# Kernel optimization log

Hardware: AMD Instinct MI355X
Metric: run time of the kernel (lower is better)

The kernel has to match this reference:

```python
import jax, jax.numpy as jnp
import numpy as np

H = W = 14
SENT = H * W  # sentinel label for background (> any real label)
DROP_THR = 0.3
STRIDE = 32


def _min_pool_3x3(labels):
    # labels: [B, H, W] int32; 8-connected neighborhood min (incl. self)
    p = jnp.pad(labels, ((0, 0), (1, 1), (1, 1)), constant_values=SENT)
    shifts = [p[:, i:i + H, j:j + W] for i in range(3) for j in range(3)]
    return jnp.min(jnp.stack(shifts, axis=0), axis=0)


def _label_components(mask):
    # mask: [B, H, W] bool. Iterative min-label propagation (8-connectivity,
    # matching skimage.measure.label default for 2D arrays).
    init = jnp.where(mask, jnp.arange(H * W, dtype=jnp.int32).reshape(1, H, W), SENT)

    def step(_, lab):
        return jnp.where(mask, jnp.minimum(lab, _min_pool_3x3(lab)), SENT)

    # H*W iterations is a safe upper bound on the longest propagation path
    return jax.lax.fori_loop(0, H * W, step, init)


def reference(fms):
    # fms: [B, C, 14, 14]
    attention = jnp.mean(fms, axis=1)                      # [B, H, W] (channel mean)
    max_val = jnp.max(attention.reshape(attention.shape[0], -1), axis=1)  # [B]
    mask = attention > (max_val * DROP_THR)[:, None, None]  # threshold mask

    labels = _label_components(mask)                       # [B, H, W]

    # per-label pixel counts (areas); label ids in [0, H*W)
    lab_flat = labels.reshape(labels.shape[0], -1)          # [B, HW]
    counts = jnp.sum(lab_flat[:, :, None] == jnp.arange(H * W)[None, None, :], axis=1)  # [B, HW]
    # first max -> smallest label id, matching areas.index(max(areas)) in raster order
    best = jnp.argmax(counts, axis=1)                       # [B]
    sel = labels == best[:, None, None]                     # [B, H, W] largest component

    idx = jnp.arange(H)
    row_any = sel.any(axis=2)                               # [B, H]
    col_any = sel.any(axis=1)                               # [B, W]
    min_row = jnp.min(jnp.where(row_any, idx, H), axis=1)
    max_row = jnp.max(jnp.where(row_any, idx, -1), axis=1) + 1  # exclusive, skimage bbox
    min_col = jnp.min(jnp.where(col_any, idx, W), axis=1)
    max_col = jnp.max(jnp.where(col_any, idx, -1), axis=1) + 1

    # empty-mask fallback -> full-image bbox [0, 0, 14, 14]
    empty = jnp.max(counts, axis=1) == 0
    min_row = jnp.where(empty, 0, min_row)
    min_col = jnp.where(empty, 0, min_col)
    max_row = jnp.where(empty, H, max_row)
    max_col = jnp.where(empty, W, max_col)

    x0 = jnp.maximum(min_row * STRIDE - 1, 0)
    y0 = jnp.maximum(min_col * STRIDE - 1, 0)
    x1 = max_row * STRIDE - 1
    y1 = max_col * STRIDE - 1
    return jnp.stack([x0, y0, x1, y1], axis=1).astype(jnp.int32)  # [B, 4]


def setup_inputs() -> dict:
    key = jax.random.key(0)
    fms = jax.random.uniform(key, (64, 2048, 14, 14), dtype=jnp.float32)
    return {"fms": fms}
```

## Files before the change

### kernel.cpp

```cpp
#include <hip/hip_runtime.h>

#define HH 14
#define WW 14
#define P 196
#define CTOT 2048
#define NCHUNK 16
#define CCHUNK 128
#define Q4 49

__global__ __launch_bounds__(256) void chansum_kernel(const float* __restrict__ fms,
                                                      float* __restrict__ partials) {
    const int blk = blockIdx.x;
    const int b = blk >> 4;
    const int k = blk & 15;
    const float4* __restrict__ base =
        (const float4*)(fms + ((size_t)b * CTOT + (size_t)k * CCHUNK) * P);

    __shared__ float lds[5 * P];
    const int t = threadIdx.x;

    if (t < 5 * Q4) {
        const int q = t % Q4;
        const int r = t / Q4;
        float4 acc = {0.f, 0.f, 0.f, 0.f};
        #pragma unroll 4
        for (int c = r; c < CCHUNK; c += 5) {
            float4 v = base[c * Q4 + q];
            acc.x += v.x; acc.y += v.y; acc.z += v.z; acc.w += v.w;
        }
        const int o = r * P + q * 4;
        lds[o + 0] = acc.x; lds[o + 1] = acc.y;
        lds[o + 2] = acc.z; lds[o + 3] = acc.w;
    }
    __syncthreads();
    if (t < P) {
        float s = lds[t] + lds[P + t] + lds[2 * P + t] + lds[3 * P + t] + lds[4 * P + t];
        partials[(size_t)blk * P + t] = s;
    }
}

__global__ __launch_bounds__(256) void bbox_kernel(const float* __restrict__ partials,
                                                   int* __restrict__ out) {
    const int b = blockIdx.x;
    const int t = threadIdx.x;

    __shared__ float redf[4];
    __shared__ unsigned long long ball[4];

    float a = -1e30f;
    if (t < P) {
        const float* pb = partials + (size_t)b * NCHUNK * P + t;
        a = 0.f;
        #pragma unroll
        for (int k = 0; k < NCHUNK; ++k) a += pb[k * P];
    }

    float mx = a;
    #pragma unroll
    for (int off = 32; off >= 1; off >>= 1) mx = fmaxf(mx, __shfl_xor(mx, off));
    if ((t & 63) == 0) redf[t >> 6] = mx;
    __syncthreads();
    const float maxv = fmaxf(fmaxf(redf[0], redf[1]), fmaxf(redf[2], redf[3]));

    const bool maskp = (t < P) && (a > maxv * 0.3f);
    const unsigned long long wb = __ballot(maskp);
    if ((t & 63) == 0) ball[t >> 6] = wb;
    __syncthreads();
    if (t >= 64) return;

    const unsigned long long B0 = ball[0], B1 = ball[1], B2 = ball[2], B3 = ball[3];

    if (B0 == ~0ull && B1 == ~0ull && B2 == ~0ull && (B3 & 0xFull) == 0xFull) {
        if (t == 0) {
            out[b * 4 + 0] = 0;
            out[b * 4 + 1] = 0;
            out[b * 4 + 2] = HH * 32 - 1;
            out[b * 4 + 3] = WW * 32 - 1;
        }
        return;
    }

    const int l = t;
    unsigned rem = 0;
    if (l < HH) {
        const int start = WW * l, w = start >> 6, off = start & 63;
        const unsigned long long Barr[4] = {B0, B1, B2, B3};
        unsigned long long v = Barr[w] >> off;
        if (off + WW > 64) v |= Barr[w + 1] << (64 - off);
        rem = (unsigned)v & 0x3FFFu;
    }

    unsigned bestRow = 0;
    int bestA = 0;

    for (;;) {
        const unsigned long long rb = __ballot(rem != 0);
        if (rb == 0) break;
        const int sr = __ffsll(rb) - 1;
        unsigned reach = (l == sr) ? (rem & (unsigned)(-(int)rem)) : 0u;

        for (;;) {
            const unsigned h = reach | (reach << 1) | (reach >> 1);
            const unsigned up = __shfl_up(h, 1);
            const unsigned dn = __shfl_down(h, 1);
            const unsigned nv = (h | up | dn) & rem;
            const bool chg = (nv != reach);
            reach = nv;
            if (!__any(chg)) break;
        }

        int area = __popc(reach);
        #pragma unroll
        for (int off = 32; off >= 1; off >>= 1) area += __shfl_xor(area, off);
        if (area > bestA) { bestA = area; bestRow = reach; }
        rem &= ~reach;
    }

    int mnr, mxr, mnc, mxc;
    if (bestA == 0) {
        mnr = 0; mxr = HH - 1; mnc = 0; mxc = WW - 1;
    } else {
        const unsigned long long rowb = __ballot(bestRow != 0);
        mnr = __ffsll(rowb) - 1;
        mxr = 63 - __clzll(rowb);
        unsigned cols = bestRow;
        #pragma unroll
        for (int off = 32; off >= 1; off >>= 1) cols |= __shfl_xor(cols, off);
        mnc = __ffs(cols) - 1;
        mxc = 31 - __clz(cols);
    }
    if (l == 0) {
        out[b * 4 + 0] = max(mnr * 32 - 1, 0);
        out[b * 4 + 1] = max(mnc * 32 - 1, 0);
        out[b * 4 + 2] = (mxr + 1) * 32 - 1;
        out[b * 4 + 3] = (mxc + 1) * 32 - 1;
    }
}

extern "C" void kernel_launch(void* const* d_in, const int* in_sizes, int n_in,
                              void* d_out, int out_size, void* d_ws, size_t ws_size,
                              hipStream_t stream) {
    const float* fms = (const float*)d_in[0];
    int* out = (int*)d_out;
    float* partials = (float*)d_ws;

    chansum_kernel<<<dim3(64 * NCHUNK), dim3(256), 0, stream>>>(fms, partials);
    bbox_kernel<<<dim3(64), dim3(256), 0, stream>>>(partials, out);
}
```

Baseline: 22.67 us.

## Fuse channel-sum and bbox kernels via last-block atomic counter

```diff
diff --git a/kernel.cpp b/kernel.cpp
--- a/kernel.cpp
+++ b/kernel.cpp
@@ -8,8 +8,14 @@
 #define CCHUNK 128
 #define Q4 49
 
-__global__ __launch_bounds__(256) void chansum_kernel(const float* __restrict__ fms,
-                                                      float* __restrict__ partials) {
+
+typedef unsigned long long u64;
+union pk2 { float2 f; u64 u; };
+
+__global__ __launch_bounds__(256) void fused_kernel(const float* __restrict__ fms,
+                                                    unsigned* __restrict__ counters,
+                                                    float* __restrict__ partials,
+                                                    int* __restrict__ out) {
     const int blk = blockIdx.x;
     const int b = blk >> 4;
     const int k = blk & 15;
@@ -17,6 +23,11 @@
         (const float4*)(fms + ((size_t)b * CTOT + (size_t)k * CCHUNK) * P);
 
     __shared__ float lds[5 * P];
+    __shared__ float att[P];
+    __shared__ float redf[4];
+    __shared__ unsigned long long ball[4];
+    __shared__ unsigned oldv;
+
     const int t = threadIdx.x;
 
     if (t < 5 * Q4) {
@@ -33,27 +44,36 @@
         lds[o + 2] = acc.z; lds[o + 3] = acc.w;
     }
     __syncthreads();
-    if (t < P) {
-        float s = lds[t] + lds[P + t] + lds[2 * P + t] + lds[3 * P + t] + lds[4 * P + t];
-        partials[(size_t)blk * P + t] = s;
+    if (t < P / 2) {
+        const int p0 = 2 * t;
+        pk2 v;
+        v.f.x = lds[p0]     + lds[P + p0]     + lds[2 * P + p0]     + lds[3 * P + p0]     + lds[4 * P + p0];
+        v.f.y = lds[p0 + 1] + lds[P + p0 + 1] + lds[2 * P + p0 + 1] + lds[3 * P + p0 + 1] + lds[4 * P + p0 + 1];
+        __hip_atomic_store((u64*)(partials + (size_t)blk * P) + t, v.u,
+                           __ATOMIC_RELAXED, __HIP_MEMORY_SCOPE_AGENT);
     }
-}
+    asm volatile("s_waitcnt vmcnt(0)" ::: "memory");
+    __syncthreads();
+    if (t == 0)
+        oldv = __hip_atomic_fetch_add(&counters[b], 1u,
+                                      __ATOMIC_RELAXED, __HIP_MEMORY_SCOPE_AGENT);
+    __syncthreads();
+    if ((oldv & 15u) != 15u) return;
 
-__global__ __launch_bounds__(256) void bbox_kernel(const float* __restrict__ partials,
-                                                   int* __restrict__ out) {
-    const int b = blockIdx.x;
-    const int t = threadIdx.x;
+    if (t < P / 2) {
+        const u64* pb = (const u64*)(partials + (size_t)b * NCHUNK * P) + t;
+        float2 acc = {0.f, 0.f};
+        #pragma unroll
+        for (int kk = 0; kk < NCHUNK; ++kk) {
+            pk2 v;
+            v.u = __hip_atomic_load(pb + kk * (P / 2), __ATOMIC_RELAXED, __HIP_MEMORY_SCOPE_AGENT);
+            acc.x += v.f.x; acc.y += v.f.y;
+        }
+        att[2 * t] = acc.x; att[2 * t + 1] = acc.y;
+    }
+    __syncthreads();
 
-    __shared__ float redf[4];
-    __shared__ unsigned long long ball[4];
-
-    float a = -1e30f;
-    if (t < P) {
-        const float* pb = partials + (size_t)b * NCHUNK * P + t;
-        a = 0.f;
-        #pragma unroll
-        for (int k = 0; k < NCHUNK; ++k) a += pb[k * P];
-    }
+    const float a = (t < P) ? att[t] : -1e30f;
 
     float mx = a;
     #pragma unroll
@@ -142,8 +162,8 @@
                               hipStream_t stream) {
     const float* fms = (const float*)d_in[0];
     int* out = (int*)d_out;
-    float* partials = (float*)d_ws;
+    unsigned* counters = (unsigned*)d_ws;
+    float* partials = (float*)((char*)d_ws + 256);
 
-    chansum_kernel<<<dim3(64 * NCHUNK), dim3(256), 0, stream>>>(fms, partials);
-    bbox_kernel<<<dim3(64), dim3(256), 0, stream>>>(partials, out);
+    fused_kernel<<<dim3(64 * NCHUNK), dim3(256), 0, stream>>>(fms, counters, partials, out);
 }
```

Measured after the change: 24.56 us. 1.08x slower.
